# Kernel optimization log

Hardware: AMD Instinct MI355X
Metric: run time of the kernel (lower is better)

Reference implementation:

```python
import jax, jax.numpy as jnp
import numpy as np

B, N, K = 4, 16384, 8
NF = [8, 32, 64, 128, 256]
E = N * K


def setup_inputs() -> dict:
    key = jax.random.key(0)
    ks = jax.random.split(key, 16)
    x = jax.random.normal(ks[0], (B, N, NF[0]), jnp.float32)
    # knn-style edge list: every node appears as a center K times (no empty segments)
    centers = jnp.tile(jnp.repeat(jnp.arange(N), K)[None, None, :], (B, 1, 1))
    neighbors = jax.random.randint(ks[1], (B, 1, E), 0, N)
    edge_index = jnp.concatenate([centers, neighbors], axis=1)
    specs = [("0a", NF[0], NF[1]), ("0b", NF[0], NF[1]),
             ("1a", NF[1], NF[2]), ("1b", NF[1], NF[2]),
             ("2a", NF[2], NF[3]), ("2b", NF[2], NF[3]),
             ("3a", NF[3], NF[4]), ("3b", NF[3], NF[4]),
             ("cat", NF[1] + NF[2] + NF[3] + NF[4], 1)]
    inp = {"x": x, "edge_index": edge_index}
    for i, (nm, ci, co) in enumerate(specs):
        inp["W" + nm] = jax.random.normal(ks[2 + i], (ci, co), jnp.float32) / np.sqrt(ci)
        inp["g" + nm] = jnp.ones((co,), jnp.float32)   # BN gamma
        inp["b" + nm] = jnp.zeros((co,), jnp.float32)  # BN beta
    inp["bias"] = jnp.zeros((1,), jnp.float32)
    return inp


def _bn(x, g, b):
    # training-mode BatchNorm1d over all rows (GraphBatchNorm1d reduces over batch*num_points)
    m = x.mean(0)
    v = jnp.mean(jnp.square(x - m), 0)  # biased variance, as torch BN uses for normalization
    return g * (x - m) * jax.lax.rsqrt(v + 1e-5) + b


def _mlp(x, W, g, b):
    # Linear(bias=False) -> BN -> LeakyReLU(0.2)
    return jax.nn.leaky_relu(_bn(x @ W, g, b), negative_slope=0.2)


def reference(x, edge_index,
              W0a, g0a, b0a, W0b, g0b, b0b,
              W1a, g1a, b1a, W1b, g1b, b1b,
              W2a, g2a, b2a, W2b, g2b, b2b,
              W3a, g3a, b3a, W3b, g3b, b3b,
              Wcat, gcat, bcat, bias):
    BN = B * N
    xf = x.reshape(BN, NF[0])
    ei = edge_index.transpose(1, 0, 2).reshape(2, -1)  # [2, B*E]
    off = jnp.repeat(jnp.arange(B) * N, E)
    centers = ei[0] + off
    neighbors = ei[1] + off
    segmax = lambda v: jax.ops.segment_max(v, centers, num_segments=BN)
    x0 = _mlp(xf, W0a, g0a, b0a) + segmax(_mlp(xf[neighbors] - xf[centers], W0b, g0b, b0b))
    x1 = _mlp(x0, W1a, g1a, b1a) + segmax(_mlp(x0, W1b, g1b, b1b)[neighbors])
    x2 = _mlp(x1, W2a, g2a, b2a) + segmax(_mlp(x1, W2b, g2b, b2b)[neighbors])
    x3 = _mlp(x2, W3a, g3a, b3a) + segmax(_mlp(x2, W3b, g3b, b3b)[neighbors])
    x_cat = _mlp(jnp.concatenate([x0, x1, x2, x3], axis=-1), Wcat, gcat, bcat)
    return x_cat + bias
```

## Files before the change

### kernel.cpp

```cpp
#include <hip/hip_runtime.h>
#include <math.h>

static constexpr int BB = 4;
static constexpr int NN = 16384;
static constexpr int KK = 8;
static constexpr int EE = 131072;
static constexpr int RR = 65536;
static constexpr int EG = 524288;

static constexpr int SPL = 64;
static constexpr size_t SLOT = (size_t)SPL*512;

static constexpr size_t OFF_X0 = 0;
static constexpr size_t OFF_X1 = OFF_X0 + (size_t)RR*32;
static constexpr size_t OFF_X2 = OFF_X1 + (size_t)RR*64;
static constexpr size_t OFF_X3 = OFF_X2 + (size_t)RR*128;
static constexpr size_t OFF_ZB = OFF_X3 + (size_t)RR*256;
static constexpr size_t OFF_ZC = OFF_ZB + (size_t)RR*128;
static constexpr size_t OFF_S  = OFF_ZC + (size_t)RR;
static constexpr size_t OFF_WP = OFF_S + 9*SLOT;
static constexpr size_t WP1_OFF = 0;
static constexpr size_t WP2_OFF = 4096;
static constexpr size_t WP3_OFF = 4096 + 16384;

__device__ __forceinline__ float lrelu(float x) { return fmaxf(x, 0.2f*x); }

__device__ __forceinline__ unsigned short f2h(float f) {
    _Float16 h = (_Float16)f;
    return *(unsigned short*)&h;
}
__device__ __forceinline__ float h2f(unsigned short u) {
    _Float16 h = *(_Float16*)&u;
    return (float)h;
}

typedef __attribute__((ext_vector_type(8))) _Float16 half8v;
typedef __attribute__((ext_vector_type(8))) unsigned short ushort8v;
typedef __attribute__((ext_vector_type(4))) float float4v;

__global__ __launch_bounds__(256) void k_l0_node(const float* __restrict__ xf,
                                                 const float* __restrict__ W,
                                                 unsigned short* __restrict__ z,
                                                 float* __restrict__ S) {
    __shared__ float w[256];
    __shared__ float red[64];
    int tid = threadIdx.x;
    w[tid] = W[tid];
    if (tid < 64) red[tid] = 0.f;
    __syncthreads();
    int r = blockIdx.x*256 + tid;
    const float4* xr = (const float4*)(xf + (size_t)r*8);
    float4 a = xr[0], b = xr[1];
    float xv[8] = {a.x,a.y,a.z,a.w,b.x,b.y,b.z,b.w};
    float op[32];
#pragma unroll
    for (int c = 0; c < 32; ++c) {
        float s = 0.f;
#pragma unroll
        for (int k = 0; k < 8; ++k) s = fmaf(xv[k], w[k*32+c], s);
        op[c] = s;
    }
    ushort8v* zp = (ushort8v*)(z + (size_t)r*32);
#pragma unroll
    for (int i = 0; i < 4; ++i) {
        ushort8v h;
#pragma unroll
        for (int j = 0; j < 8; ++j) h[j] = f2h(op[i*8+j]);
        zp[i] = h;
    }
#pragma unroll
    for (int c = 0; c < 32; ++c) {
        float s = op[c], q = op[c]*op[c];
#pragma unroll
        for (int off = 32; off >= 1; off >>= 1) {
            s += __shfl_xor(s, off, 64);
            q += __shfl_xor(q, off, 64);
        }
        if ((tid & 63) == 0) { atomicAdd(&red[c], s); atomicAdd(&red[32+c], q); }
    }
    __syncthreads();
    if (tid < 64) atomicAdd(&S[(size_t)(blockIdx.x & (SPL-1))*512 + tid], red[tid]);
}

__global__ __launch_bounds__(256) void k_edge_stats(const float* __restrict__ xf,
                                                    const int* __restrict__ ei,
                                                    const float* __restrict__ W,
                                                    float* __restrict__ S) {
    __shared__ float w[256];
    __shared__ float red[64];
    int tid = threadIdx.x;
    w[tid] = W[tid];
    if (tid < 64) red[tid] = 0.f;
    __syncthreads();
    int g = tid & 3;
    int cg = g*8;
    float s[8], q[8];
#pragma unroll
    for (int j = 0; j < 8; ++j) { s[j] = 0.f; q[j] = 0.f; }
    int qid = (blockIdx.x*256 + tid) >> 2;
    int NQ = (gridDim.x*256) >> 2;
    for (int e = qid; e < EG; e += NQ) {
        int b = e >> 17, jj = e & (EE-1);
        const int* base = ei + (size_t)b*2*EE;
        int ctr = base[jj], nbr = base[EE + jj];
        const float4* pc = (const float4*)(xf + ((size_t)(b<<14) + ctr)*8);
        const float4* pn = (const float4*)(xf + ((size_t)(b<<14) + nbr)*8);
        float4 c0 = pc[0], c1 = pc[1], n0 = pn[0], n1 = pn[1];
        float d[8] = {n0.x-c0.x, n0.y-c0.y, n0.z-c0.z, n0.w-c0.w,
                      n1.x-c1.x, n1.y-c1.y, n1.z-c1.z, n1.w-c1.w};
#pragma unroll
        for (int j = 0; j < 8; ++j) {
            int c = cg + j;
            float z = 0.f;
#pragma unroll
            for (int k = 0; k < 8; ++k) z = fmaf(d[k], w[k*32+c], z);
            s[j] += z; q[j] = fmaf(z, z, q[j]);
        }
    }
#pragma unroll
    for (int off = 4; off <= 32; off <<= 1) {
#pragma unroll
        for (int j = 0; j < 8; ++j) {
            s[j] += __shfl_xor(s[j], off, 64);
            q[j] += __shfl_xor(q[j], off, 64);
        }
    }
    if ((tid & 63) < 4) {
#pragma unroll
        for (int j = 0; j < 8; ++j) {
            atomicAdd(&red[cg + j], s[j]);
            atomicAdd(&red[32 + cg + j], q[j]);
        }
    }
    __syncthreads();
    if (tid < 64) atomicAdd(&S[(size_t)(blockIdx.x & (SPL-1))*512 + tid], red[tid]);
}

__global__ __launch_bounds__(256) void k_edge_apply(const float* __restrict__ xf,
                                                    const int* __restrict__ ei,
                                                    const float* __restrict__ W,
                                                    const float* __restrict__ Sa,
                                                    const float* __restrict__ Sb,
                                                    const float* __restrict__ ga,
                                                    const float* __restrict__ ba,
                                                    const float* __restrict__ gb,
                                                    const float* __restrict__ bbp,
                                                    const float* __restrict__ Wc,
                                                    unsigned short* __restrict__ x0,
                                                    float* __restrict__ zc) {
    __shared__ float w[256];
    __shared__ float scbA[32], sgnb[32], shb[32], sca[32], sha[32], swc[32];
    int tid = threadIdx.x;
    w[tid] = W[tid];
    if (tid < 32) {
        float su = 0.f, qu = 0.f;
        for (int p = 0; p < SPL; ++p) { su += Sa[(size_t)p*512 + tid]; qu += Sa[(size_t)p*512 + 32 + tid]; }
        float m = su*(1.f/RR);
        float v = fmaxf(qu*(1.f/RR) - m*m, 0.f);
        float sc = ga[tid]*rsqrtf(v + 1e-5f);
        sca[tid] = sc; sha[tid] = fmaf(-m, sc, ba[tid]);
        swc[tid] = Wc[tid];
    } else if (tid < 64) {
        int c = tid - 32;
        float su = 0.f, qu = 0.f;
        for (int p = 0; p < SPL; ++p) { su += Sb[(size_t)p*512 + c]; qu += Sb[(size_t)p*512 + 32 + c]; }
        float m = su*(1.f/EG);
        float v = fmaxf(qu*(1.f/EG) - m*m, 0.f);
        float sc = gb[c]*rsqrtf(v + 1e-5f);
        scbA[c] = fabsf(sc); sgnb[c] = (sc >= 0.f) ? 1.f : -1.f;
        shb[c] = fmaf(-m, sc, bbp[c]);
    }
    __syncthreads();
    int r = blockIdx.x*256 + tid;
    int b = r >> 14, n = r & (NN-1);
    const int4* nb4 = (const int4*)(ei + (size_t)b*2*EE + EE + n*KK);
    int4 q0 = nb4[0], q1 = nb4[1];
    int nbr[KK] = {q0.x,q0.y,q0.z,q0.w,q1.x,q1.y,q1.z,q1.w};
    const float4* pc = (const float4*)(xf + (size_t)r*8);
    float4 c0 = pc[0], c1 = pc[1];
    float mx[32];
#pragma unroll
    for (int c = 0; c < 32; ++c) mx[c] = -3.0e38f;
    for (int k = 0; k < KK; ++k) {
        int j = nbr[k];
        const float4* pn = (const float4*)(xf + ((size_t)(b<<14) + j)*8);
        float4 n0 = pn[0], n1 = pn[1];
        float d[8] = {n0.x-c0.x, n0.y-c0.y, n0.z-c0.z, n0.w-c0.w,
                      n1.x-c1.x, n1.y-c1.y, n1.z-c1.z, n1.w-c1.w};
#pragma unroll
        for (int c = 0; c < 32; ++c) {
            float z = 0.f;
#pragma unroll
            for (int k2 = 0; k2 < 8; ++k2) z = fmaf(d[k2], w[k2*32+c], z);
            mx[c] = fmaxf(mx[c], sgnb[c]*z);
        }
    }
    ushort8v* xp = (ushort8v*)(x0 + (size_t)r*32);
    float sdot = 0.f;
#pragma unroll
    for (int i = 0; i < 4; ++i) {
        ushort8v v = xp[i];
        ushort8v o;
#pragma unroll
        for (int j = 0; j < 8; ++j) {
            int c = i*8 + j;
            float y = lrelu(fmaf(mx[c], scbA[c], shb[c]));
            float val = lrelu(fmaf(h2f(v[j]), sca[c], sha[c])) + y;
            o[j] = f2h(val);
            sdot = fmaf(val, swc[c], sdot);
        }
        xp[i] = o;
    }
    zc[r] = sdot;
}

template<int CI, int CO>
__device__ __forceinline__ void packone(int t, const float* __restrict__ Wa,
                                        const float* __restrict__ Wb,
                                        unsigned short* __restrict__ Wp) {
    constexpr int NT = 2*CO;
    constexpr int KT = CI/32;
    int ng = t % NT, k = t / NT;
    float v = (ng < CO) ? Wa[(size_t)k*CO + ng] : Wb[(size_t)k*CO + (ng - CO)];
    int nt = ng >> 4, n = ng & 15;
    int kt = k >> 5, kq = (k & 31) >> 3, j = k & 7;
    int f = nt*KT + kt;
    int idx = f*512 + ((kq*16 + n)<<3) + j;
    Wp[idx] = f2h(v);
}

__global__ __launch_bounds__(256) void k_prep(const float* __restrict__ W1a, const float* __restrict__ W1b,
                                              const float* __restrict__ W2a, const float* __restrict__ W2b,
                                              const float* __restrict__ W3a, const float* __restrict__ W3b,
                                              unsigned short* __restrict__ wp1,
                                              unsigned short* __restrict__ wp2,
                                              unsigned short* __restrict__ wp3,
                                              float* __restrict__ S) {
    int t = blockIdx.x*256 + threadIdx.x;
    int NT_ = gridDim.x*256;
    for (int u = t; u < (int)(9*SLOT); u += NT_) S[u] = 0.f;
    for (int u = t; u < 32*128;  u += NT_) packone<32,64>(u, W1a, W1b, wp1);
    for (int u = t; u < 64*256;  u += NT_) packone<64,128>(u, W2a, W2b, wp2);
    for (int u = t; u < 128*512; u += NT_) packone<128,256>(u, W3a, W3b, wp3);
}

template<int CI, int CO, int MW>
__global__ __launch_bounds__(256, MW) void k_mfma_dual4(const unsigned short* __restrict__ X,
                                                        const unsigned short* __restrict__ Wp,
                                                        unsigned short* __restrict__ Za,
                                                        unsigned short* __restrict__ Zb,
                                                        float* __restrict__ Sa,
                                                        float* __restrict__ Sb) {
    constexpr int NCH = 4;
    constexpr int KT = CI/32;
    constexpr int WCNT = NCH*KT*512;
    constexpr int ROWT = RR/64;
    constexpr int STR = NCH*16 + 8;
    constexpr int XW  = (CI < 64) ? CI : 64;
    constexpr int PLB = CO/64;
    __shared__ unsigned short scr[4][16*STR];
    int tid = threadIdx.x;
    int lane = tid & 63, wid = tid >> 6;
    int ch = blockIdx.y;
    int wglob = blockIdx.x*4 + wid;
    int NW = gridDim.x*4;
    int n = lane & 15, kq = lane >> 4;
    int rg = lane >> 3, c8l = (lane & 7)*8;
    unsigned short* myscr = scr[wid];
    size_t pl = (size_t)(wglob & (SPL-1)) * 512;
    bool isA = (ch < PLB);
    unsigned short* Zp = (isA ? Za : Zb) + (size_t)(isA ? ch : ch - PLB)*((size_t)RR*64);

    half8v wreg[KT][NCH];
    {
        const unsigned short* Wc = Wp + (size_t)ch*WCNT;
#pragma unroll
        for (int kt = 0; kt < KT; ++kt)
#pragma unroll
            for (int j = 0; j < NCH; ++j)
                wreg[kt][j] = *(const half8v*)&Wc[(j*KT + kt)*512 + lane*8];
    }

    float4v ps[NCH], pq[NCH];
#pragma unroll
    for (int j = 0; j < NCH; ++j) { ps[j] = (float4v){0,0,0,0}; pq[j] = (float4v){0,0,0,0}; }

    auto issue = [&](half8v (&dst)[4], size_t rowb, int kt) {
        int k0 = kt*32 + kq*8;
        int xpl = k0 >> 6;
        int xoff = k0 & (XW-1);
        const unsigned short* Xp = X + (size_t)xpl*((size_t)RR*64);
#pragma unroll
        for (int i = 0; i < 4; ++i)
            dst[i] = *(const half8v*)&Xp[(rowb + i*16 + n)*XW + xoff];
    };

    auto epilogue = [&](float4v (&acc)[4][NCH], size_t rowbase) {
#pragma unroll
        for (int j = 0; j < NCH; ++j)
#pragma unroll
            for (int i = 0; i < 4; ++i) {
                float4v a4 = acc[i][j];
#pragma unroll
                for (int reg = 0; reg < 4; ++reg) {
                    ps[j][reg] += a4[reg];
                    pq[j][reg] = fmaf(a4[reg], a4[reg], pq[j][reg]);
                }
            }
#pragma unroll
        for (int i = 0; i < 4; ++i) {
            __builtin_amdgcn_wave_barrier();
#pragma unroll
            for (int j = 0; j < NCH; ++j) {
                float4v a4 = acc[i][j];
                ushort4 h = { f2h(a4[0]), f2h(a4[1]), f2h(a4[2]), f2h(a4[3]) };
                *(ushort4*)&myscr[n*STR + j*16 + kq*4] = h;
            }
            __builtin_amdgcn_wave_barrier();
#pragma unroll
            for (int i2 = 0; i2 < 2; ++i2) {
                int rit = rg + i2*8;
                ushort8v v = *(const ushort8v*)&myscr[rit*STR + c8l];
                *(ushort8v*)&Zp[(rowbase + i*16 + rit)*64 + c8l] = v;
            }
        }
    };

    if constexpr (KT == 1) {
        for (int t = wglob; t < ROWT; t += NW) {
            size_t rowbase = (size_t)t*64;
            float4v acc[4][NCH];
#pragma unroll
            for (int i = 0; i < 4; ++i)
#pragma unroll
                for (int j = 0; j < NCH; ++j) acc[i][j] = (float4v){0,0,0,0};
            half8v b[4];
            issue(b, rowbase, 0);
#pragma unroll
            for (int j = 0; j < NCH; ++j)
#pragma unroll
                for (int i = 0; i < 4; ++i)
                    acc[i][j] = __builtin_amdgcn_mfma_f32_16x16x32_f16(wreg[0][j], b[i], acc[i][j], 0, 0, 0);
            epilogue(acc, rowbase);
        }
    } else {
        half8v b0[4], b1[4];
        int t = wglob;
        if (t < ROWT) issue(b0, (size_t)t*64, 0);
        for (; t < ROWT; t += NW) {
            size_t rowbase = (size_t)t*64;
            int t2 = t + NW;
            size_t nextrb = (t2 < ROWT) ? (size_t)t2*64 : rowbase;
            float4v acc[4][NCH];
#pragma unroll
            for (int i = 0; i < 4; ++i)
#pragma unroll
                for (int j = 0; j < NCH; ++j) acc[i][j] = (float4v){0,0,0,0};

            auto step = [&](half8v (&bc)[4], half8v (&bn)[4], int kt) {
                if (kt + 1 < KT) issue(bn, rowbase, kt + 1);
                else             issue(bn, nextrb, 0);
#pragma unroll
                for (int j = 0; j < NCH; ++j)
#pragma unroll
                    for (int i = 0; i < 4; ++i)
                        acc[i][j] = __builtin_amdgcn_mfma_f32_16x16x32_f16(wreg[kt][j], bc[i], acc[i][j], 0, 0, 0);
            };
#pragma unroll
            for (int kh = 0; kh < KT/2; ++kh) {
                step(b0, b1, 2*kh);
                step(b1, b0, 2*kh + 1);
            }
            epilogue(acc, rowbase);
        }
    }

    {
        float* Sg = isA ? Sa : Sb;
        int cb0 = isA ? ch*64 : ch*64 - CO;
#pragma unroll
        for (int j = 0; j < NCH; ++j) {
#pragma unroll
            for (int reg = 0; reg < 4; ++reg) {
                float s = ps[j][reg], q = pq[j][reg];
                s += __shfl_xor(s, 1, 64); q += __shfl_xor(q, 1, 64);
                s += __shfl_xor(s, 2, 64); q += __shfl_xor(q, 2, 64);
                s += __shfl_xor(s, 4, 64); q += __shfl_xor(q, 4, 64);
                s += __shfl_xor(s, 8, 64); q += __shfl_xor(q, 8, 64);
                if (n == 0) {
                    int col = cb0 + j*16 + kq*4 + reg;
                    atomicAdd(&Sg[pl + col], s);
                    atomicAdd(&Sg[pl + CO + col], q);
                }
            }
        }
    }
}

template<int CO>
__global__ __launch_bounds__(256) void k_redstats(float* __restrict__ Sa,
                                                  float* __restrict__ Sb) {
    int t = blockIdx.x*256 + threadIdx.x;
    for (int u = t; u < 2*CO; u += gridDim.x*256) {
        float sa = 0.f, sb = 0.f;
        for (int p = 1; p < SPL; ++p) {
            sa += Sa[(size_t)p*512 + u];
            sb += Sb[(size_t)p*512 + u];
        }
        Sa[u] += sa;
        Sb[u] += sb;
    }
}

template<int CO, bool WRITEBACK>
__global__ __launch_bounds__(256) void k_gathermax(unsigned short* __restrict__ xi,
                                                   const unsigned short* __restrict__ zbh,
                                                   const int* __restrict__ ei,
                                                   const float* __restrict__ Sa,
                                                   const float* __restrict__ Sb,
                                                   const float* __restrict__ ga,
                                                   const float* __restrict__ ba,
                                                   const float* __restrict__ gb,
                                                   const float* __restrict__ bbp,
                                                   const float* __restrict__ Wc,
                                                   int wcoff,
                                                   float* __restrict__ zc) {
    constexpr int CQ = CO/8;
    __shared__ float sca[CO], sha[CO], sbA[CO], shb[CO], swc[CO], sgn[CO];
    int tid = threadIdx.x;
    for (int u = tid; u < CO; u += 256) {
        float m = Sa[u]*(1.f/RR);
        float v = fmaxf(Sa[CO+u]*(1.f/RR) - m*m, 0.f);
        float sc = ga[u]*rsqrtf(v + 1e-5f);
        sca[u] = sc; sha[u] = fmaf(-m, sc, ba[u]);
        m = Sb[u]*(1.f/RR);
        v = fmaxf(Sb[CO+u]*(1.f/RR) - m*m, 0.f);
        sc = gb[u]*rsqrtf(v + 1e-5f);
        sbA[u] = fabsf(sc); sgn[u] = (sc >= 0.f) ? 1.f : -1.f;
        shb[u] = fmaf(-m, sc, bbp[u]);
        swc[u] = Wc[wcoff + u];
    }
    __syncthreads();
    int bx = (int)((blockIdx.x & 7)*(gridDim.x >> 3) + (blockIdx.x >> 3));
    int t = bx*256 + tid;
    int r = t / CQ;
    int c8 = (t % CQ)*8;
    int pln = c8 >> 6;
    int off = c8 & 63;
    const unsigned short* zpl = zbh + (size_t)pln*((size_t)RR*64);
    unsigned short* xpl = xi + (size_t)pln*((size_t)RR*64);
    int b = r >> 14, n = r & (NN-1);
    const int4* nb4 = (const int4*)(ei + (size_t)b*2*EE + EE + n*KK);
    int4 q0 = nb4[0], q1 = nb4[1];
    int nbr[KK] = {q0.x,q0.y,q0.z,q0.w,q1.x,q1.y,q1.z,q1.w};
    size_t bb64 = ((size_t)(b<<14))*64 + off;
    ushort8v* xp = (ushort8v*)&xpl[(size_t)r*64 + off];
    ushort8v a = *xp;
    ushort8v u[KK];
#pragma unroll
    for (int k = 0; k < KK; ++k)
        u[k] = *(const ushort8v*)(zpl + bb64 + (size_t)nbr[k]*64);
    float sg[8], sb[8], hb[8];
#pragma unroll
    for (int j = 0; j < 8; ++j) { sg[j] = sgn[c8+j]; sb[j] = sbA[c8+j]; hb[j] = shb[c8+j]; }
    float mx[8];
#pragma unroll
    for (int j = 0; j < 8; ++j) mx[j] = -3e38f;
#pragma unroll
    for (int k = 0; k < KK; ++k)
#pragma unroll
        for (int j = 0; j < 8; ++j)
            mx[j] = fmaxf(mx[j], sg[j]*h2f(u[k][j]));
    float sdot = 0.f;
    if (WRITEBACK) {
        ushort8v o;
#pragma unroll
        for (int j = 0; j < 8; ++j) {
            int c = c8 + j;
            float y = lrelu(fmaf(mx[j], sb[j], hb[j]));
            float val = lrelu(fmaf(h2f(a[j]), sca[c], sha[c])) + y;
            o[j] = f2h(val);
            sdot = fmaf(val, swc[c], sdot);
        }
        *xp = o;
    } else {
#pragma unroll
        for (int j = 0; j < 8; ++j) {
            int c = c8 + j;
            float y = lrelu(fmaf(mx[j], sb[j], hb[j]));
            float val = lrelu(fmaf(h2f(a[j]), sca[c], sha[c])) + y;
            sdot = fmaf(val, swc[c], sdot);
        }
    }
#pragma unroll
    for (int w = CQ/2; w >= 1; w >>= 1) sdot += __shfl_xor(sdot, w, 64);
    int lane = tid & 63;
    if ((lane & (CQ-1)) == 0) atomicAdd(&zc[r], sdot);
}

__global__ __launch_bounds__(256) void k_catstats(const float* __restrict__ zc,
                                                  float* __restrict__ S8) {
    __shared__ float rs2[2];
    int tid = threadIdx.x;
    if (tid < 2) rs2[tid] = 0.f;
    __syncthreads();
    float v = zc[blockIdx.x*256 + tid];
    float s = v, q = v*v;
#pragma unroll
    for (int off = 32; off >= 1; off >>= 1) {
        s += __shfl_xor(s, off, 64);
        q += __shfl_xor(q, off, 64);
    }
    if ((tid & 63) == 0) { atomicAdd(&rs2[0], s); atomicAdd(&rs2[1], q); }
    __syncthreads();
    if (tid == 0) {
        int p = blockIdx.x & 255;
        atomicAdd(&S8[p*2],     rs2[0]);
        atomicAdd(&S8[p*2 + 1], rs2[1]);
    }
}

__global__ __launch_bounds__(256) void k_catfinal(const float* __restrict__ zc,
                                                  const float* __restrict__ S8,
                                                  const float* __restrict__ g,
                                                  const float* __restrict__ bb,
                                                  const float* __restrict__ bias,
                                                  float* __restrict__ out) {
    __shared__ float rs[256], rq[256];
    int tid = threadIdx.x;
    rs[tid] = S8[tid*2];
    rq[tid] = S8[tid*2 + 1];
    __syncthreads();
#pragma unroll
    for (int h = 128; h >= 1; h >>= 1) {
        if (tid < h) { rs[tid] += rs[tid+h]; rq[tid] += rq[tid+h]; }
        __syncthreads();
    }
    int r = blockIdx.x*256 + tid;
    const float invR = 1.f/65536.f;
    float m = rs[0]*invR;
    float v = fmaxf(rq[0]*invR - m*m, 0.f);
    float sc = g[0]*rsqrtf(v + 1e-5f);
    float sh = fmaf(-m, sc, bb[0]);
    float y = lrelu(fmaf(zc[r], sc, sh));
    out[r] = y + bias[0];
}

extern "C" void kernel_launch(void* const* d_in, const int* in_sizes, int n_in,
                              void* d_out, int out_size, void* d_ws, size_t ws_size,
                              hipStream_t stream) {
    const float* x    = (const float*)d_in[0];
    const int*   ei   = (const int*)d_in[1];
    const float* W0a  = (const float*)d_in[2];
    const float* g0a  = (const float*)d_in[3];
    const float* b0a  = (const float*)d_in[4];
    const float* W0b  = (const float*)d_in[5];
    const float* g0b  = (const float*)d_in[6];
    const float* b0b  = (const float*)d_in[7];
    const float* W1a  = (const float*)d_in[8];
    const float* g1a  = (const float*)d_in[9];
    const float* b1a  = (const float*)d_in[10];
    const float* W1b  = (const float*)d_in[11];
    const float* g1b  = (const float*)d_in[12];
    const float* b1b  = (const float*)d_in[13];
    const float* W2a  = (const float*)d_in[14];
    const float* g2a  = (const float*)d_in[15];
    const float* b2a  = (const float*)d_in[16];
    const float* W2b  = (const float*)d_in[17];
    const float* g2b  = (const float*)d_in[18];
    const float* b2b  = (const float*)d_in[19];
    const float* W3a  = (const float*)d_in[20];
    const float* g3a  = (const float*)d_in[21];
    const float* b3a  = (const float*)d_in[22];
    const float* W3b  = (const float*)d_in[23];
    const float* g3b  = (const float*)d_in[24];
    const float* b3b  = (const float*)d_in[25];
    const float* Wcat = (const float*)d_in[26];
    const float* gcat = (const float*)d_in[27];
    const float* bcat = (const float*)d_in[28];
    const float* bias = (const float*)d_in[29];
    float* out = (float*)d_out;

    float* ws = (float*)d_ws;
    unsigned short* x0 = (unsigned short*)(ws + OFF_X0);
    unsigned short* x1 = (unsigned short*)(ws + OFF_X1);
    unsigned short* x2 = (unsigned short*)(ws + OFF_X2);
    unsigned short* x3 = (unsigned short*)(ws + OFF_X3);
    unsigned short* zbh = (unsigned short*)(ws + OFF_ZB);
    float* zc = ws + OFF_ZC;
    float* S  = ws + OFF_S;
    unsigned short* wpbase = (unsigned short*)(ws + OFF_WP);
    unsigned short* wp1 = wpbase + WP1_OFF;
    unsigned short* wp2 = wpbase + WP2_OFF;
    unsigned short* wp3 = wpbase + WP3_OFF;
    auto Sl = [&](int i) { return S + (size_t)i*SLOT; };

    k_prep<<<256, 256, 0, stream>>>(W1a, W1b, W2a, W2b, W3a, W3b, wp1, wp2, wp3, S);

    k_l0_node<<<RR/256, 256, 0, stream>>>(x, W0a, x0, Sl(0));
    k_edge_stats<<<512, 256, 0, stream>>>(x, ei, W0b, Sl(1));
    k_edge_apply<<<RR/256, 256, 0, stream>>>(x, ei, W0b, Sl(0), Sl(1),
                                             g0a, b0a, g0b, b0b, Wcat, x0, zc);

    k_mfma_dual4<32,64,3><<<dim3(256,2), 256, 0, stream>>>(x0, wp1, x1, zbh, Sl(2), Sl(3));
    k_redstats<64><<<4, 256, 0, stream>>>(Sl(2), Sl(3));
    k_gathermax<64,true><<<RR*8/256, 256, 0, stream>>>(x1, zbh, ei, Sl(2), Sl(3),
                                                       g1a, b1a, g1b, b1b, Wcat, 32, zc);

    k_mfma_dual4<64,128,3><<<dim3(128,4), 256, 0, stream>>>(x1, wp2, x2, zbh, Sl(4), Sl(5));
    k_redstats<128><<<4, 256, 0, stream>>>(Sl(4), Sl(5));
    k_gathermax<128,true><<<RR*16/256, 256, 0, stream>>>(x2, zbh, ei, Sl(4), Sl(5),
                                                         g2a, b2a, g2b, b2b, Wcat, 96, zc);

    k_mfma_dual4<128,256,2><<<dim3(64,8), 256, 0, stream>>>(x2, wp3, x3, zbh, Sl(6), Sl(7));
    k_redstats<256><<<4, 256, 0, stream>>>(Sl(6), Sl(7));
    k_gathermax<256,false><<<RR*32/256, 256, 0, stream>>>(x3, zbh, ei, Sl(6), Sl(7),
                                                          g3a, b3a, g3b, b3b, Wcat, 224, zc);

    k_catstats<<<RR/256, 256, 0, stream>>>(zc, Sl(8));
    k_catfinal<<<RR/256, 256, 0, stream>>>(zc, Sl(8), gcat, bcat, bias, out);
}
```

Measured before the change: 298.1 us.

## Fuse layer-0 node MLP, edge stats and edge max into one kernel

Replaces the separate layer-0 node kernel, edge-statistics kernel and edge-apply kernel with one fused kernel. It computes the node projection, the edge BN sums and the sign-adjusted per-channel neighbor max in a single pass over the neighbor gathers, using four threads per node. The pre-BN max is stored in a new fp32 workspace buffer, and a lightweight apply kernel finishes normalization and the residual. This removes one full gather pass and one launch, but adds an 8 MB intermediate write and read and relies on the workspace being large enough.

```diff
diff --git a/kernel.cpp b/kernel.cpp
--- a/kernel.cpp
+++ b/kernel.cpp
@@ -19,6 +19,7 @@
 static constexpr size_t OFF_ZC = OFF_ZB + (size_t)RR*128;
 static constexpr size_t OFF_S  = OFF_ZC + (size_t)RR;
 static constexpr size_t OFF_WP = OFF_S + 9*SLOT;
+static constexpr size_t OFF_MX = OFF_WP + 65536;
 static constexpr size_t WP1_OFF = 0;
 static constexpr size_t WP2_OFF = 4096;
 static constexpr size_t WP3_OFF = 4096 + 16384;
@@ -38,120 +39,122 @@
 typedef __attribute__((ext_vector_type(8))) unsigned short ushort8v;
 typedef __attribute__((ext_vector_type(4))) float float4v;
 
-__global__ __launch_bounds__(256) void k_l0_node(const float* __restrict__ xf,
-                                                 const float* __restrict__ W,
-                                                 unsigned short* __restrict__ z,
-                                                 float* __restrict__ S) {
-    __shared__ float w[256];
-    __shared__ float red[64];
+__global__ __launch_bounds__(256) void k_l0_fused(const float* __restrict__ xf,
+                                                  const int* __restrict__ ei,
+                                                  const float* __restrict__ Wa,
+                                                  const float* __restrict__ Wb,
+                                                  const float* __restrict__ gb,
+                                                  unsigned short* __restrict__ xa,
+                                                  float* __restrict__ mxb,
+                                                  float* __restrict__ Sa,
+                                                  float* __restrict__ Sb) {
+    __shared__ float wa[256], wb[256];
+    __shared__ float red[128];
+    __shared__ float sgns[32];
     int tid = threadIdx.x;
-    w[tid] = W[tid];
-    if (tid < 64) red[tid] = 0.f;
+    wa[tid] = Wa[tid];
+    wb[tid] = Wb[tid];
+    if (tid < 128) red[tid] = 0.f;
+    if (tid < 32) sgns[tid] = (gb[tid] >= 0.f) ? 1.f : -1.f;
     __syncthreads();
-    int r = blockIdx.x*256 + tid;
-    const float4* xr = (const float4*)(xf + (size_t)r*8);
-    float4 a = xr[0], b = xr[1];
-    float xv[8] = {a.x,a.y,a.z,a.w,b.x,b.y,b.z,b.w};
-    float op[32];
-#pragma unroll
-    for (int c = 0; c < 32; ++c) {
+    int g = tid & 3, cg = g*8;
+    int r = (blockIdx.x*256 + tid) >> 2;
+    int b = r >> 14, n = r & (NN-1);
+    const int4* nb4 = (const int4*)(ei + (size_t)b*2*EE + EE + n*KK);
+    int4 q0v = nb4[0], q1v = nb4[1];
+    int nbr[KK] = {q0v.x,q0v.y,q0v.z,q0v.w,q1v.x,q1v.y,q1v.z,q1v.w};
+    const float4* pc = (const float4*)(xf + (size_t)r*8);
+    float4 c0 = pc[0], c1 = pc[1];
+    float xv[8] = {c0.x,c0.y,c0.z,c0.w,c1.x,c1.y,c1.z,c1.w};
+    float sgn[8];
+#pragma unroll
+    for (int j = 0; j < 8; ++j) sgn[j] = sgns[cg+j];
+
+    float4 nA[KK], nB[KK];
+#pragma unroll
+    for (int k = 0; k < KK; ++k) {
+        const float4* pn = (const float4*)(xf + ((size_t)(b<<14) + nbr[k])*8);
+        nA[k] = pn[0]; nB[k] = pn[1];
+    }
+
+    float opa[8];
+#pragma unroll
+    for (int j = 0; j < 8; ++j) {
         float s = 0.f;
 #pragma unroll
-        for (int k = 0; k < 8; ++k) s = fmaf(xv[k], w[k*32+c], s);
-        op[c] = s;
-    }
-    ushort8v* zp = (ushort8v*)(z + (size_t)r*32);
-#pragma unroll
-    for (int i = 0; i < 4; ++i) {
+        for (int k = 0; k < 8; ++k) s = fmaf(xv[k], wa[k*32+cg+j], s);
+        opa[j] = s;
+    }
+    {
         ushort8v h;
 #pragma unroll
-        for (int j = 0; j < 8; ++j) h[j] = f2h(op[i*8+j]);
-        zp[i] = h;
-    }
-#pragma unroll
-    for (int c = 0; c < 32; ++c) {
-        float s = op[c], q = op[c]*op[c];
-#pragma unroll
-        for (int off = 32; off >= 1; off >>= 1) {
-            s += __shfl_xor(s, off, 64);
-            q += __shfl_xor(q, off, 64);
-        }
-        if ((tid & 63) == 0) { atomicAdd(&red[c], s); atomicAdd(&red[32+c], q); }
+        for (int j = 0; j < 8; ++j) h[j] = f2h(opa[j]);
+        *(ushort8v*)&xa[(size_t)r*32 + cg] = h;
+    }
+
+    float s8[8], q8[8], mx[8];
+#pragma unroll
+    for (int j = 0; j < 8; ++j) { s8[j] = 0.f; q8[j] = 0.f; mx[j] = -3.0e38f; }
+#pragma unroll
+    for (int k = 0; k < KK; ++k) {
+        float4 n0 = nA[k], n1 = nB[k];
+        float d[8] = {n0.x-xv[0], n0.y-xv[1], n0.z-xv[2], n0.w-xv[3],
+                      n1.x-xv[4], n1.y-xv[5], n1.z-xv[6], n1.w-xv[7]};
+#pragma unroll
+        for (int jj = 0; jj < 8; ++jj) {
+            float z = 0.f;
+#pragma unroll
+            for (int k2 = 0; k2 < 8; ++k2) z = fmaf(d[k2], wb[k2*32+cg+jj], z);
+            s8[jj] += z;
+            q8[jj] = fmaf(z, z, q8[jj]);
+            mx[jj] = fmaxf(mx[jj], sgn[jj]*z);
+        }
+    }
+    {
+        float4* mp = (float4*)&mxb[(size_t)r*32 + cg];
+        mp[0] = (float4){mx[0],mx[1],mx[2],mx[3]};
+        mp[1] = (float4){mx[4],mx[5],mx[6],mx[7]};
+    }
+    float sa8[8], qa8[8];
+#pragma unroll
+    for (int j = 0; j < 8; ++j) { sa8[j] = opa[j]; qa8[j] = opa[j]*opa[j]; }
+#pragma unroll
+    for (int off = 4; off <= 32; off <<= 1) {
+#pragma unroll
+        for (int j = 0; j < 8; ++j) {
+            s8[j]  += __shfl_xor(s8[j],  off, 64);
+            q8[j]  += __shfl_xor(q8[j],  off, 64);
+            sa8[j] += __shfl_xor(sa8[j], off, 64);
+            qa8[j] += __shfl_xor(qa8[j], off, 64);
+        }
+    }
+    if ((tid & 63) < 4) {
+#pragma unroll
+        for (int j = 0; j < 8; ++j) {
+            atomicAdd(&red[cg + j],       sa8[j]);
+            atomicAdd(&red[32 + cg + j],  qa8[j]);
+            atomicAdd(&red[64 + cg + j],  s8[j]);
+            atomicAdd(&red[96 + cg + j],  q8[j]);
+        }
     }
     __syncthreads();
-    if (tid < 64) atomicAdd(&S[(size_t)(blockIdx.x & (SPL-1))*512 + tid], red[tid]);
-}
-
-__global__ __launch_bounds__(256) void k_edge_stats(const float* __restrict__ xf,
-                                                    const int* __restrict__ ei,
-                                                    const float* __restrict__ W,
-                                                    float* __restrict__ S) {
-    __shared__ float w[256];
-    __shared__ float red[64];
+    size_t pl = (size_t)(blockIdx.x & (SPL-1))*512;
+    if (tid < 64) atomicAdd(&Sa[pl + tid], red[tid]);
+    else if (tid < 128) atomicAdd(&Sb[pl + (tid - 64)], red[tid]);
+}
+
+__global__ __launch_bounds__(256) void k_edge_apply2(const float* __restrict__ mxb,
+                                                     const float* __restrict__ Sa,
+                                                     const float* __restrict__ Sb,
+                                                     const float* __restrict__ ga,
+                                                     const float* __restrict__ ba,
+                                                     const float* __restrict__ gb,
+                                                     const float* __restrict__ bbp,
+                                                     const float* __restrict__ Wc,
+                                                     unsigned short* __restrict__ x0,
+                                                     float* __restrict__ zc) {
+    __shared__ float scbA[32], shb[32], sca[32], sha[32], swc[32];
     int tid = threadIdx.x;
-    w[tid] = W[tid];
-    if (tid < 64) red[tid] = 0.f;
-    __syncthreads();
-    int g = tid & 3;
-    int cg = g*8;
-    float s[8], q[8];
-#pragma unroll
-    for (int j = 0; j < 8; ++j) { s[j] = 0.f; q[j] = 0.f; }
-    int qid = (blockIdx.x*256 + tid) >> 2;
-    int NQ = (gridDim.x*256) >> 2;
-    for (int e = qid; e < EG; e += NQ) {
-        int b = e >> 17, jj = e & (EE-1);
-        const int* base = ei + (size_t)b*2*EE;
-        int ctr = base[jj], nbr = base[EE + jj];
-        const float4* pc = (const float4*)(xf + ((size_t)(b<<14) + ctr)*8);
-        const float4* pn = (const float4*)(xf + ((size_t)(b<<14) + nbr)*8);
-        float4 c0 = pc[0], c1 = pc[1], n0 = pn[0], n1 = pn[1];
-        float d[8] = {n0.x-c0.x, n0.y-c0.y, n0.z-c0.z, n0.w-c0.w,
-                      n1.x-c1.x, n1.y-c1.y, n1.z-c1.z, n1.w-c1.w};
-#pragma unroll
-        for (int j = 0; j < 8; ++j) {
-            int c = cg + j;
-            float z = 0.f;
-#pragma unroll
-            for (int k = 0; k < 8; ++k) z = fmaf(d[k], w[k*32+c], z);
-            s[j] += z; q[j] = fmaf(z, z, q[j]);
-        }
-    }
-#pragma unroll
-    for (int off = 4; off <= 32; off <<= 1) {
-#pragma unroll
-        for (int j = 0; j < 8; ++j) {
-            s[j] += __shfl_xor(s[j], off, 64);
-            q[j] += __shfl_xor(q[j], off, 64);
-        }
-    }
-    if ((tid & 63) < 4) {
-#pragma unroll
-        for (int j = 0; j < 8; ++j) {
-            atomicAdd(&red[cg + j], s[j]);
-            atomicAdd(&red[32 + cg + j], q[j]);
-        }
-    }
-    __syncthreads();
-    if (tid < 64) atomicAdd(&S[(size_t)(blockIdx.x & (SPL-1))*512 + tid], red[tid]);
-}
-
-__global__ __launch_bounds__(256) void k_edge_apply(const float* __restrict__ xf,
-                                                    const int* __restrict__ ei,
-                                                    const float* __restrict__ W,
-                                                    const float* __restrict__ Sa,
-                                                    const float* __restrict__ Sb,
-                                                    const float* __restrict__ ga,
-                                                    const float* __restrict__ ba,
-                                                    const float* __restrict__ gb,
-                                                    const float* __restrict__ bbp,
-                                                    const float* __restrict__ Wc,
-                                                    unsigned short* __restrict__ x0,
-                                                    float* __restrict__ zc) {
-    __shared__ float w[256];
-    __shared__ float scbA[32], sgnb[32], shb[32], sca[32], sha[32], swc[32];
-    int tid = threadIdx.x;
-    w[tid] = W[tid];
     if (tid < 32) {
         float su = 0.f, qu = 0.f;
         for (int p = 0; p < SPL; ++p) { su += Sa[(size_t)p*512 + tid]; qu += Sa[(size_t)p*512 + 32 + tid]; }
@@ -167,44 +170,24 @@
         float m = su*(1.f/EG);
         float v = fmaxf(qu*(1.f/EG) - m*m, 0.f);
         float sc = gb[c]*rsqrtf(v + 1e-5f);
-        scbA[c] = fabsf(sc); sgnb[c] = (sc >= 0.f) ? 1.f : -1.f;
+        scbA[c] = fabsf(sc);
         shb[c] = fmaf(-m, sc, bbp[c]);
     }
     __syncthreads();
     int r = blockIdx.x*256 + tid;
-    int b = r >> 14, n = r & (NN-1);
-    const int4* nb4 = (const int4*)(ei + (size_t)b*2*EE + EE + n*KK);
-    int4 q0 = nb4[0], q1 = nb4[1];
-    int nbr[KK] = {q0.x,q0.y,q0.z,q0.w,q1.x,q1.y,q1.z,q1.w};
-    const float4* pc = (const float4*)(xf + (size_t)r*8);
-    float4 c0 = pc[0], c1 = pc[1];
-    float mx[32];
-#pragma unroll
-    for (int c = 0; c < 32; ++c) mx[c] = -3.0e38f;
-    for (int k = 0; k < KK; ++k) {
-        int j = nbr[k];
-        const float4* pn = (const float4*)(xf + ((size_t)(b<<14) + j)*8);
-        float4 n0 = pn[0], n1 = pn[1];
-        float d[8] = {n0.x-c0.x, n0.y-c0.y, n0.z-c0.z, n0.w-c0.w,
-                      n1.x-c1.x, n1.y-c1.y, n1.z-c1.z, n1.w-c1.w};
-#pragma unroll
-        for (int c = 0; c < 32; ++c) {
-            float z = 0.f;
-#pragma unroll
-            for (int k2 = 0; k2 < 8; ++k2) z = fmaf(d[k2], w[k2*32+c], z);
-            mx[c] = fmaxf(mx[c], sgnb[c]*z);
-        }
-    }
     ushort8v* xp = (ushort8v*)(x0 + (size_t)r*32);
+    const float4* mp = (const float4*)(mxb + (size_t)r*32);
     float sdot = 0.f;
 #pragma unroll
     for (int i = 0; i < 4; ++i) {
         ushort8v v = xp[i];
+        float4 m0 = mp[i*2], m1 = mp[i*2+1];
+        float mx8[8] = {m0.x,m0.y,m0.z,m0.w,m1.x,m1.y,m1.z,m1.w};
         ushort8v o;
 #pragma unroll
         for (int j = 0; j < 8; ++j) {
             int c = i*8 + j;
-            float y = lrelu(fmaf(mx[c], scbA[c], shb[c]));
+            float y = lrelu(fmaf(mx8[j], scbA[c], shb[c]));
             float val = lrelu(fmaf(h2f(v[j]), sca[c], sha[c])) + y;
             o[j] = f2h(val);
             sdot = fmaf(val, swc[c], sdot);
@@ -593,14 +576,14 @@
     unsigned short* wp1 = wpbase + WP1_OFF;
     unsigned short* wp2 = wpbase + WP2_OFF;
     unsigned short* wp3 = wpbase + WP3_OFF;
+    float* mxb = ws + OFF_MX;
     auto Sl = [&](int i) { return S + (size_t)i*SLOT; };
 
     k_prep<<<256, 256, 0, stream>>>(W1a, W1b, W2a, W2b, W3a, W3b, wp1, wp2, wp3, S);
 
-    k_l0_node<<<RR/256, 256, 0, stream>>>(x, W0a, x0, Sl(0));
-    k_edge_stats<<<512, 256, 0, stream>>>(x, ei, W0b, Sl(1));
-    k_edge_apply<<<RR/256, 256, 0, stream>>>(x, ei, W0b, Sl(0), Sl(1),
-                                             g0a, b0a, g0b, b0b, Wcat, x0, zc);
+    k_l0_fused<<<RR*4/256, 256, 0, stream>>>(x, ei, W0a, W0b, g0b, x0, mxb, Sl(0), Sl(1));
+    k_edge_apply2<<<RR/256, 256, 0, stream>>>(mxb, Sl(0), Sl(1),
+                                              g0a, b0a, g0b, b0b, Wcat, x0, zc);
 
     k_mfma_dual4<32,64,3><<<dim3(256,2), 256, 0, stream>>>(x0, wp1, x1, zbh, Sl(2), Sl(3));
     k_redstats<64><<<4, 256, 0, stream>>>(Sl(2), Sl(3));
```

After: 276.0 us. -7.4%, faster.
